# Performance work log

Hardware: AMD Instinct MI355X
Metric: run time of the kernel (lower is better)

## Reference

```python
import jax, jax.numpy as jnp
import numpy as np

NUM_EMB = 8192
EMB_DIM = 512
COMMITMENT_COST = 0.25
TEMPERATURE = 1.0
ENTROPY_WEIGHT = 0.1


def setup_inputs() -> dict:
    key = jax.random.key(0)
    k1, k2 = jax.random.split(key)
    z = jax.random.normal(k1, (32768, EMB_DIM), dtype=jnp.float32)
    W = jax.random.normal(k2, (NUM_EMB, EMB_DIM), dtype=jnp.float32) * 0.1
    return {"z": z, "W": W}


def reference(z, W):
    # pairwise squared distances [B, K] (scaled by temperature)
    distances = (jnp.sum(z * z, axis=1, keepdims=True)
                 + jnp.sum(W * W, axis=1)
                 - 2.0 * z @ W.T) / TEMPERATURE
    indices = jnp.argmin(distances, axis=1)          # [B]
    quantized = W[indices]                            # [B, D] gather

    commitment_loss = jnp.mean((z - jax.lax.stop_gradient(quantized)) ** 2)
    codebook_loss = jnp.mean((quantized - jax.lax.stop_gradient(z)) ** 2)

    # entropy loss over code assignment histogram
    counts = jnp.zeros((NUM_EMB,), jnp.float32).at[indices].add(1.0)
    probs = counts / jnp.maximum(counts.sum(), 1.0)
    entropy = -jnp.sum(probs * jnp.log(probs + 1e-10))
    max_entropy = jnp.log(jnp.float32(NUM_EMB))
    entropy_loss = 1.0 - entropy / max_entropy

    loss = codebook_loss + COMMITMENT_COST * commitment_loss + ENTROPY_WEIGHT * entropy_loss

    # straight-through estimator
    quantized_st = z + jax.lax.stop_gradient(quantized - z)
    return quantized_st, loss, indices
```

## Files before the change

kernel.cpp:

```cpp
#include <hip/hip_runtime.h>
#include <math.h>

#define B_ROWS 32768
#define D_DIM  512
#define K_EMB  8192

#define BMT 128
#define BNT 128
#define RSPLIT 16
#define KRANGE_R (K_EMB / RSPLIT)
#define EPS 0.10f

typedef __attribute__((ext_vector_type(4))) float f32x4;
typedef __attribute__((ext_vector_type(8))) short bf16x8;

#define GLL16(gp, lp)                                                          \
  __builtin_amdgcn_global_load_lds(                                            \
      (const __attribute__((address_space(1))) void*)(gp),                     \
      (__attribute__((address_space(3))) void*)(lp), 16, 0, 0)

__device__ __forceinline__ unsigned bf_rne(float x) {
  unsigned u = __float_as_uint(x);
  return (u + 0x7fffu + ((u >> 16) & 1u)) >> 16;
}

__global__ __launch_bounds__(256) void prep_kernel(
    const float* __restrict__ X, short* __restrict__ hi,
    short* __restrict__ lo, float* __restrict__ sq, int nrows) {
  const int wave = threadIdx.x >> 6;
  const int lane = threadIdx.x & 63;
  const int row = blockIdx.x * 4 + wave;
  if (row >= nrows) return;
  const float* xr = X + (size_t)row * D_DIM;
  float4 x0 = ((const float4*)xr)[lane * 2];
  float4 x1 = ((const float4*)xr)[lane * 2 + 1];
  float xs[8] = {x0.x, x0.y, x0.z, x0.w, x1.x, x1.y, x1.z, x1.w};
  union { short s[8]; int4 v; } H, L;
  float ssum = 0.f;
  #pragma unroll
  for (int j = 0; j < 8; ++j) {
    unsigned rh = bf_rne(xs[j]);
    H.s[j] = (short)rh;
    float h = __uint_as_float(rh << 16);
    L.s[j] = (short)bf_rne(xs[j] - h);
    ssum += xs[j] * xs[j];
  }
  *(int4*)(hi + (size_t)row * D_DIM + lane * 8) = H.v;
  *(int4*)(lo + (size_t)row * D_DIM + lane * 8) = L.v;
  #pragma unroll
  for (int o = 32; o > 0; o >>= 1) ssum += __shfl_xor(ssum, o, 64);
  if (lane == 0) sq[row] = ssum;
}

__global__ __launch_bounds__(512, 2) void stage1_kernel(
    const short* __restrict__ zhi, const short* __restrict__ whi,
    const float* __restrict__ wsq, float* __restrict__ cv1,
    int* __restrict__ ci1, float* __restrict__ cv2) {
  __shared__ short Zt[65536];
  float* rv1 = (float*)Zt;
  int*   ri1 = (int*)(Zt + 16384);
  float* rv2 = (float*)(Zt + 32768);

  const int tid = threadIdx.x;
  const int lane = tid & 63;
  const int wave = tid >> 6;
  const int wm = wave >> 2;
  const int wn = wave & 3;
  const int l15 = lane & 15, l4 = lane >> 4;
  const int row0 = blockIdx.x * 128;

  #pragma unroll
  for (int j = 0; j < 16; ++j) {
    const int slot = j * 512 + tid;
    const int r = slot & 127, dc = slot >> 7;
    GLL16(zhi + (size_t)(row0 + r) * D_DIM + dc * 8, Zt + (size_t)slot * 8);
  }

  const short* pb[4];
  #pragma unroll
  for (int cb = 0; cb < 4; ++cb)
    pb[cb] = whi + (size_t)(wn * 64 + cb * 16 + l15) * D_DIM + l4 * 8;

  float v1[16], v2[16];
  int   i1[16];
  #pragma unroll
  for (int s = 0; s < 16; ++s) { v1[s] = INFINITY; v2[s] = INFINITY; i1[s] = 0x7fffffff; }

  bf16x8 bcur[4];
  #pragma unroll
  for (int cb = 0; cb < 4; ++cb) bcur[cb] = *(const bf16x8*)(pb[cb]);

  __syncthreads();

  for (int kt = 0; kt < K_EMB; kt += 256) {
    f32x4 acc[4][4];
    #pragma unroll
    for (int rb = 0; rb < 4; ++rb)
      #pragma unroll
      for (int cb = 0; cb < 4; ++cb) acc[rb][cb] = (f32x4)0.f;

    #pragma unroll 4
    for (int dc = 0; dc < 16; ++dc) {
      const int nt0 = (dc == 15) ? kt + 256 : kt;
      const int nt = (nt0 < K_EMB) ? nt0 : 0;
      const int nd = (dc == 15) ? 0 : (dc + 1) * 32;
      const size_t noff = (size_t)nt * D_DIM + nd;
      bf16x8 bnxt[4];
      #pragma unroll
      for (int cb = 0; cb < 4; ++cb) bnxt[cb] = *(const bf16x8*)(pb[cb] + noff);

      bf16x8 a[4];
      #pragma unroll
      for (int rb = 0; rb < 4; ++rb)
        a[rb] = *(const bf16x8*)&Zt[((dc * 4 + l4) * 128 + wm * 64 + rb * 16 + l15) * 8];
      #pragma unroll
      for (int rb = 0; rb < 4; ++rb)
        #pragma unroll
        for (int cb = 0; cb < 4; ++cb)
          acc[rb][cb] = __builtin_amdgcn_mfma_f32_16x16x32_bf16(
              a[rb], bcur[cb], acc[rb][cb], 0, 0, 0);
      #pragma unroll
      for (int cb = 0; cb < 4; ++cb) bcur[cb] = bnxt[cb];
    }

    #pragma unroll
    for (int cb = 0; cb < 4; ++cb) {
      const int col = kt + wn * 64 + cb * 16 + l15;
      const float wv = wsq[col];
      #pragma unroll
      for (int rb = 0; rb < 4; ++rb) {
        f32x4 a = acc[rb][cb];
        #pragma unroll
        for (int rg = 0; rg < 4; ++rg) {
          const float dist = wv - 2.0f * a[rg];
          const int s = rb * 4 + rg;
          if (dist < v1[s]) {
            v2[s] = v1[s]; v1[s] = dist; i1[s] = col;
          } else {
            v2[s] = fminf(v2[s], dist);
          }
        }
      }
    }
  }

  __syncthreads();
  #pragma unroll
  for (int rb = 0; rb < 4; ++rb)
    #pragma unroll
    for (int rg = 0; rg < 4; ++rg) {
      const int s = rb * 4 + rg;
      const int R = wm * 64 + rb * 16 + l4 * 4 + rg;
      const int c = wn * 16 + l15;
      rv1[R * 64 + c] = v1[s];
      ri1[R * 64 + c] = i1[s];
      rv2[R * 64 + c] = v2[s];
    }
  __syncthreads();

  if (tid < 128) {
    float V1 = INFINITY, V2 = INFINITY;
    int I1 = 0x7fffffff;
    #pragma unroll 8
    for (int t = 0; t < 64; ++t) {
      const float a1 = rv1[tid * 64 + t];
      const int ai = ri1[tid * 64 + t];
      const float a2 = rv2[tid * 64 + t];
      if (a1 < V1 || (a1 == V1 && ai < I1)) {
        V2 = fminf(V1, a2); V1 = a1; I1 = ai;
      } else {
        V2 = fminf(V2, a1);
      }
    }
    cv1[row0 + tid] = V1; ci1[row0 + tid] = I1; cv2[row0 + tid] = V2;
  }
}

__global__ __launch_bounds__(256) void merge_flag_kernel(
    const float* __restrict__ cv1, const int* __restrict__ ci1,
    const float* __restrict__ cv2, int* __restrict__ idx,
    float* __restrict__ out_idx_f, int* __restrict__ hist,
    unsigned long long* __restrict__ packed, int* __restrict__ cnt,
    int* __restrict__ list) {
  const int row = blockIdx.x * 256 + threadIdx.x;
  const float V1 = cv1[row];
  const int I1 = ci1[row];
  const float V2 = cv2[row];
  if (V2 - V1 >= EPS) {
    idx[row] = I1;
    out_idx_f[row] = (float)I1;
    atomicAdd(&hist[I1], 1);
  } else {
    packed[row] = 0xffffffffffffffffULL;
    const int p = atomicAdd(cnt, 1);
    list[p] = row;
  }
}

__global__ __launch_bounds__(256, 2) void refine_kernel(
    const short* __restrict__ zhi, const short* __restrict__ zlo,
    const short* __restrict__ whi, const short* __restrict__ wlo,
    const float* __restrict__ zz, const float* __restrict__ wsq,
    const int* __restrict__ cnt, const int* __restrict__ list,
    unsigned long long* __restrict__ packed) {
  __shared__ char smem[32768];
  short* Ah = (short*)smem;
  short* Al = (short*)(smem + 8192);
  short* Bh = (short*)(smem + 16384);
  short* Bl = (short*)(smem + 24576);
  float* rv = (float*)smem;
  int*   ri = (int*)(smem + 16384);

  const int n = *cnt;
  const int bx = blockIdx.x;
  const int rt = bx >> 4;
  const int ks = bx & 15;
  if (rt * BMT >= n) return;
  const int k0 = ks * KRANGE_R;

  const int tid = threadIdx.x;
  const int lane = tid & 63;
  const int wave = tid >> 6;
  const int wm = wave >> 1, wn = wave & 1;
  const int l15 = lane & 15, l4 = lane >> 4;

  const int r0s = tid & 127;
  const int kc0 = tid >> 7;
  const int kc1 = kc0 + 2;
  const int rowg = list[min(rt * BMT + r0s, n - 1)];

  float zzr[16];
  #pragma unroll
  for (int rb = 0; rb < 4; ++rb)
    #pragma unroll
    for (int rg = 0; rg < 4; ++rg) {
      const int m = wm * 64 + rb * 16 + l4 * 4 + rg;
      zzr[rb * 4 + rg] = zz[list[min(rt * BMT + m, n - 1)]];
    }

  float best[16];
  int   bidx[16];
  #pragma unroll
  for (int s = 0; s < 16; ++s) { best[s] = INFINITY; bidx[s] = 0x7fffffff; }

  for (int kt = 0; kt < KRANGE_R; kt += BNT) {
    f32x4 acc[4][4];
    #pragma unroll
    for (int rb = 0; rb < 4; ++rb)
      #pragma unroll
      for (int cb = 0; cb < 4; ++cb) acc[rb][cb] = (f32x4)0.f;

    for (int d0 = 0; d0 < D_DIM; d0 += 32) {
      const size_t ga0 = (size_t)rowg * D_DIM + d0 + kc0 * 8;
      const size_t ga1 = (size_t)rowg * D_DIM + d0 + kc1 * 8;
      const size_t gb0 = (size_t)(k0 + kt + r0s) * D_DIM + d0 + kc0 * 8;
      const size_t gb1 = (size_t)(k0 + kt + r0s) * D_DIM + d0 + kc1 * 8;
      GLL16(zhi + ga0, Ah + (size_t)tid * 8);
      GLL16(zhi + ga1, Ah + (size_t)(tid + 256) * 8);
      GLL16(zlo + ga0, Al + (size_t)tid * 8);
      GLL16(zlo + ga1, Al + (size_t)(tid + 256) * 8);
      GLL16(whi + gb0, Bh + (size_t)tid * 8);
      GLL16(whi + gb1, Bh + (size_t)(tid + 256) * 8);
      GLL16(wlo + gb0, Bl + (size_t)tid * 8);
      GLL16(wlo + gb1, Bl + (size_t)(tid + 256) * 8);
      __syncthreads();

      bf16x8 ah[4], al[4], bh[4], bl[4];
      #pragma unroll
      for (int rb = 0; rb < 4; ++rb) {
        const int m = wm * 64 + rb * 16 + l15;
        ah[rb] = *(const bf16x8*)&Ah[(l4 * 128 + m) * 8];
        al[rb] = *(const bf16x8*)&Al[(l4 * 128 + m) * 8];
      }
      #pragma unroll
      for (int cb = 0; cb < 4; ++cb) {
        const int nn = wn * 64 + cb * 16 + l15;
        bh[cb] = *(const bf16x8*)&Bh[(l4 * 128 + nn) * 8];
        bl[cb] = *(const bf16x8*)&Bl[(l4 * 128 + nn) * 8];
      }
      #pragma unroll
      for (int rb = 0; rb < 4; ++rb)
        #pragma unroll
        for (int cb = 0; cb < 4; ++cb) {
          acc[rb][cb] = __builtin_amdgcn_mfma_f32_16x16x32_bf16(
              ah[rb], bh[cb], acc[rb][cb], 0, 0, 0);
          acc[rb][cb] = __builtin_amdgcn_mfma_f32_16x16x32_bf16(
              ah[rb], bl[cb], acc[rb][cb], 0, 0, 0);
          acc[rb][cb] = __builtin_amdgcn_mfma_f32_16x16x32_bf16(
              al[rb], bh[cb], acc[rb][cb], 0, 0, 0);
        }
      __syncthreads();
    }

    #pragma unroll
    for (int cb = 0; cb < 4; ++cb) {
      const int col = k0 + kt + wn * 64 + cb * 16 + l15;
      const float wv = wsq[col];
      #pragma unroll
      for (int rb = 0; rb < 4; ++rb) {
        f32x4 a = acc[rb][cb];
        #pragma unroll
        for (int rg = 0; rg < 4; ++rg) {
          const float dist = (zzr[rb * 4 + rg] + wv) - 2.0f * a[rg];
          const int s = rb * 4 + rg;
          if (dist < best[s]) { best[s] = dist; bidx[s] = col; }
        }
      }
    }
  }

  #pragma unroll
  for (int rb = 0; rb < 4; ++rb)
    #pragma unroll
    for (int rg = 0; rg < 4; ++rg) {
      const int s = rb * 4 + rg;
      const int R = wm * 64 + rb * 16 + l4 * 4 + rg;
      rv[R * 32 + wn * 16 + l15] = best[s];
      ri[R * 32 + wn * 16 + l15] = bidx[s];
    }
  __syncthreads();

  if (tid < BMT && rt * BMT + tid < n) {
    float bv = INFINITY;
    int bi = 0x7fffffff;
    #pragma unroll
    for (int t = 0; t < 32; ++t) {
      const float v = rv[tid * 32 + t];
      const int ix = ri[tid * 32 + t];
      if (v < bv || (v == bv && ix < bi)) { bv = v; bi = ix; }
    }
    const int row = list[rt * BMT + tid];
    const unsigned long long pk =
        ((unsigned long long)__float_as_uint(bv) << 32) | (unsigned)bi;
    atomicMin(&packed[row], pk);
  }
}

__global__ __launch_bounds__(256) void final_merge_kernel(
    const int* __restrict__ cnt, const int* __restrict__ list,
    const unsigned long long* __restrict__ packed, int* __restrict__ idx,
    float* __restrict__ out_idx_f, int* __restrict__ hist) {
  const int t = blockIdx.x * 256 + threadIdx.x;
  if (t >= *cnt) return;
  const int row = list[t];
  const int bi = (int)(packed[row] & 0xffffffffULL);
  idx[row] = bi;
  out_idx_f[row] = (float)bi;
  atomicAdd(&hist[bi], 1);
}

__global__ __launch_bounds__(256) void gather_kernel(
    const float* __restrict__ z, const float* __restrict__ W,
    const int* __restrict__ idx, float* __restrict__ out,
    double* __restrict__ mse_part) {
  __shared__ float wsum[4];
  const int wave = threadIdx.x >> 6;
  const int lane = threadIdx.x & 63;
  const int row = blockIdx.x * 4 + wave;
  const int k = idx[row];
  const float* zr = z + (size_t)row * D_DIM;
  const float* wr = W + (size_t)k * D_DIM;
  float* outr = out + (size_t)row * D_DIM;
  float s = 0.f;
  #pragma unroll
  for (int h = 0; h < 2; ++h) {
    const int c = h * 256 + lane * 4;
    float4 zv = *(const float4*)(zr + c);
    float4 qv = *(const float4*)(wr + c);
    float4 st;
    st.x = zv.x + (qv.x - zv.x);
    st.y = zv.y + (qv.y - zv.y);
    st.z = zv.z + (qv.z - zv.z);
    st.w = zv.w + (qv.w - zv.w);
    float dx = zv.x - qv.x, dy = zv.y - qv.y, dz = zv.z - qv.z, dw = zv.w - qv.w;
    s += dx * dx + dy * dy + dz * dz + dw * dw;
    *(float4*)(outr + c) = st;
  }
  #pragma unroll
  for (int o = 32; o > 0; o >>= 1) s += __shfl_xor(s, o, 64);
  if (lane == 0) wsum[wave] = s;
  __syncthreads();
  if (threadIdx.x == 0)
    mse_part[blockIdx.x] =
        (double)wsum[0] + (double)wsum[1] + (double)wsum[2] + (double)wsum[3];
}

__global__ __launch_bounds__(256) void loss_kernel(
    const int* __restrict__ hist, const double* __restrict__ mse_part,
    float* __restrict__ out_loss) {
  __shared__ float ls[4];
  __shared__ double ld[4];
  const int tid = threadIdx.x;
  float e = 0.f;
  double ms = 0.0;
  for (int b = tid; b < K_EMB; b += 256) {
    float p = (float)hist[b] * (1.0f / 32768.0f);
    e += p * logf(p + 1e-10f);
    ms += mse_part[b];
  }
  #pragma unroll
  for (int o = 32; o > 0; o >>= 1) {
    e += __shfl_xor(e, o, 64);
    ms += __shfl_xor(ms, o, 64);
  }
  if ((tid & 63) == 0) { ls[tid >> 6] = e; ld[tid >> 6] = ms; }
  __syncthreads();
  if (tid == 0) {
    float entropy = -(ls[0] + ls[1] + ls[2] + ls[3]);
    float mse = (float)((ld[0] + ld[1] + ld[2] + ld[3]) / 16777216.0);
    float entropy_loss = 1.0f - entropy / logf(8192.0f);
    out_loss[0] = mse + 0.25f * mse + 0.1f * entropy_loss;
  }
}

extern "C" void kernel_launch(void* const* d_in, const int* in_sizes, int n_in,
                              void* d_out, int out_size, void* d_ws, size_t ws_size,
                              hipStream_t stream) {
  const float* z = (const float*)d_in[0];
  const float* W = (const float*)d_in[1];
  float* out = (float*)d_out;

  char* ws = (char*)d_ws;
  int*    cnt     = (int*)(ws + 8);
  int*    hist    = (int*)(ws + 4096);
  unsigned long long* packed = (unsigned long long*)(ws + 65536);
  float*  zz   = (float*)(ws + 327680);
  float*  wsq  = (float*)(ws + 458752);
  int*    idx  = (int*)(ws + 491520);
  int*    list = (int*)(ws + 622592);
  float*  cv1  = (float*)(ws + 786432);
  int*    ci1  = (int*)(ws + 1310720);
  float*  cv2  = (float*)(ws + 1835008);
  double* mse_part = (double*)(ws + 2097152);
  short*  zhi  = (short*)(ws + 4194304);
  short*  zlo  = (short*)(ws + 37748736);
  short*  whi  = (short*)(ws + 71303168);
  short*  wlo  = (short*)(ws + 79691776);

  hipMemsetAsync(d_ws, 0, 36864, stream);

  prep_kernel<<<B_ROWS / 4, 256, 0, stream>>>(z, zhi, zlo, zz, B_ROWS);
  prep_kernel<<<K_EMB / 4, 256, 0, stream>>>(W, whi, wlo, wsq, K_EMB);

  stage1_kernel<<<B_ROWS / 128, 512, 0, stream>>>(zhi, whi, wsq, cv1, ci1, cv2);

  merge_flag_kernel<<<B_ROWS / 256, 256, 0, stream>>>(
      cv1, ci1, cv2, idx, out + (size_t)B_ROWS * D_DIM + 1, hist,
      packed, cnt, list);

  refine_kernel<<<(B_ROWS / BMT) * RSPLIT, 256, 0, stream>>>(
      zhi, zlo, whi, wlo, zz, wsq, cnt, list, packed);

  final_merge_kernel<<<B_ROWS / 256, 256, 0, stream>>>(
      cnt, list, packed, idx, out + (size_t)B_ROWS * D_DIM + 1, hist);

  gather_kernel<<<B_ROWS / 4, 256, 0, stream>>>(z, W, idx, out, mse_part);

  loss_kernel<<<1, 256, 0, stream>>>(hist, mse_part,
                                     out + (size_t)B_ROWS * D_DIM);
}
```

Before: 807.0 us.

## Shrink stage1 block tile to 64 rows and reduce top-2 via wave shuffles

The stage1 distance/argmin kernel now handles 64 query rows per block instead of 128, with each of 8 waves owning 32 codebook columns per 256-column tile. This halves LDS use and accumulator registers, so launch bounds can allow 4 blocks per CU and there are twice as many blocks. The cross-lane top-2 reduction becomes a shuffle butterfly within each wave followed by a small 8-way LDS merge, replacing the large LDS scratch scan. In exchange, each block loads the W tiles for half as many rows, doubling global/L2 traffic for the codebook, and per-wave MFMA work per load drops.

```diff
diff --git a/kernel.cpp b/kernel.cpp
--- a/kernel.cpp
+++ b/kernel.cpp
@@ -52,52 +52,50 @@
   if (lane == 0) sq[row] = ssum;
 }
 
-__global__ __launch_bounds__(512, 2) void stage1_kernel(
+__global__ __launch_bounds__(512, 4) void stage1_kernel(
     const short* __restrict__ zhi, const short* __restrict__ whi,
     const float* __restrict__ wsq, float* __restrict__ cv1,
     int* __restrict__ ci1, float* __restrict__ cv2) {
-  __shared__ short Zt[65536];
+  __shared__ short Zt[32768];
   float* rv1 = (float*)Zt;
-  int*   ri1 = (int*)(Zt + 16384);
-  float* rv2 = (float*)(Zt + 32768);
+  int*   ri1 = (int*)(Zt + 1024);
+  float* rv2 = (float*)(Zt + 2048);
 
   const int tid = threadIdx.x;
   const int lane = tid & 63;
   const int wave = tid >> 6;
-  const int wm = wave >> 2;
-  const int wn = wave & 3;
   const int l15 = lane & 15, l4 = lane >> 4;
-  const int row0 = blockIdx.x * 128;
-
-  #pragma unroll
-  for (int j = 0; j < 16; ++j) {
+  const int row0 = blockIdx.x * 64;
+
+  #pragma unroll
+  for (int j = 0; j < 8; ++j) {
     const int slot = j * 512 + tid;
-    const int r = slot & 127, dc = slot >> 7;
+    const int r = slot & 63, dc = slot >> 6;
     GLL16(zhi + (size_t)(row0 + r) * D_DIM + dc * 8, Zt + (size_t)slot * 8);
   }
 
-  const short* pb[4];
-  #pragma unroll
-  for (int cb = 0; cb < 4; ++cb)
-    pb[cb] = whi + (size_t)(wn * 64 + cb * 16 + l15) * D_DIM + l4 * 8;
+  const short* pb[2];
+  #pragma unroll
+  for (int cb = 0; cb < 2; ++cb)
+    pb[cb] = whi + (size_t)(wave * 32 + cb * 16 + l15) * D_DIM + l4 * 8;
 
   float v1[16], v2[16];
   int   i1[16];
   #pragma unroll
   for (int s = 0; s < 16; ++s) { v1[s] = INFINITY; v2[s] = INFINITY; i1[s] = 0x7fffffff; }
 
-  bf16x8 bcur[4];
-  #pragma unroll
-  for (int cb = 0; cb < 4; ++cb) bcur[cb] = *(const bf16x8*)(pb[cb]);
+  bf16x8 bcur[2];
+  #pragma unroll
+  for (int cb = 0; cb < 2; ++cb) bcur[cb] = *(const bf16x8*)(pb[cb]);
 
   __syncthreads();
 
   for (int kt = 0; kt < K_EMB; kt += 256) {
-    f32x4 acc[4][4];
+    f32x4 acc[4][2];
     #pragma unroll
     for (int rb = 0; rb < 4; ++rb)
       #pragma unroll
-      for (int cb = 0; cb < 4; ++cb) acc[rb][cb] = (f32x4)0.f;
+      for (int cb = 0; cb < 2; ++cb) acc[rb][cb] = (f32x4)0.f;
 
     #pragma unroll 4
     for (int dc = 0; dc < 16; ++dc) {
@@ -105,27 +103,27 @@
       const int nt = (nt0 < K_EMB) ? nt0 : 0;
       const int nd = (dc == 15) ? 0 : (dc + 1) * 32;
       const size_t noff = (size_t)nt * D_DIM + nd;
-      bf16x8 bnxt[4];
-      #pragma unroll
-      for (int cb = 0; cb < 4; ++cb) bnxt[cb] = *(const bf16x8*)(pb[cb] + noff);
+      bf16x8 bnxt[2];
+      #pragma unroll
+      for (int cb = 0; cb < 2; ++cb) bnxt[cb] = *(const bf16x8*)(pb[cb] + noff);
 
       bf16x8 a[4];
       #pragma unroll
       for (int rb = 0; rb < 4; ++rb)
-        a[rb] = *(const bf16x8*)&Zt[((dc * 4 + l4) * 128 + wm * 64 + rb * 16 + l15) * 8];
+        a[rb] = *(const bf16x8*)&Zt[((dc * 4 + l4) * 64 + rb * 16 + l15) * 8];
       #pragma unroll
       for (int rb = 0; rb < 4; ++rb)
         #pragma unroll
-        for (int cb = 0; cb < 4; ++cb)
+        for (int cb = 0; cb < 2; ++cb)
           acc[rb][cb] = __builtin_amdgcn_mfma_f32_16x16x32_bf16(
               a[rb], bcur[cb], acc[rb][cb], 0, 0, 0);
       #pragma unroll
-      for (int cb = 0; cb < 4; ++cb) bcur[cb] = bnxt[cb];
-    }
-
-    #pragma unroll
-    for (int cb = 0; cb < 4; ++cb) {
-      const int col = kt + wn * 64 + cb * 16 + l15;
+      for (int cb = 0; cb < 2; ++cb) bcur[cb] = bnxt[cb];
+    }
+
+    #pragma unroll
+    for (int cb = 0; cb < 2; ++cb) {
+      const int col = kt + wave * 32 + cb * 16 + l15;
       const float wv = wsq[col];
       #pragma unroll
       for (int rb = 0; rb < 4; ++rb) {
@@ -146,26 +144,37 @@
 
   __syncthreads();
   #pragma unroll
-  for (int rb = 0; rb < 4; ++rb)
-    #pragma unroll
-    for (int rg = 0; rg < 4; ++rg) {
-      const int s = rb * 4 + rg;
-      const int R = wm * 64 + rb * 16 + l4 * 4 + rg;
-      const int c = wn * 16 + l15;
-      rv1[R * 64 + c] = v1[s];
-      ri1[R * 64 + c] = i1[s];
-      rv2[R * 64 + c] = v2[s];
-    }
-  __syncthreads();
-
-  if (tid < 128) {
+  for (int s = 0; s < 16; ++s) {
+    float a1 = v1[s], a2 = v2[s];
+    int ai = i1[s];
+    #pragma unroll
+    for (int m = 1; m < 16; m <<= 1) {
+      const float b1 = __shfl_xor(a1, m, 64);
+      const float b2 = __shfl_xor(a2, m, 64);
+      const int   bi = __shfl_xor(ai, m, 64);
+      if (b1 < a1 || (b1 == a1 && bi < ai)) {
+        a2 = fminf(a1, b2); a1 = b1; ai = bi;
+      } else {
+        a2 = fminf(a2, b1);
+      }
+    }
+    if (l15 == 0) {
+      const int r = (s >> 2) * 16 + l4 * 4 + (s & 3);
+      rv1[r * 8 + wave] = a1;
+      ri1[r * 8 + wave] = ai;
+      rv2[r * 8 + wave] = a2;
+    }
+  }
+  __syncthreads();
+
+  if (tid < 64) {
     float V1 = INFINITY, V2 = INFINITY;
     int I1 = 0x7fffffff;
-    #pragma unroll 8
-    for (int t = 0; t < 64; ++t) {
-      const float a1 = rv1[tid * 64 + t];
-      const int ai = ri1[tid * 64 + t];
-      const float a2 = rv2[tid * 64 + t];
+    #pragma unroll
+    for (int w = 0; w < 8; ++w) {
+      const float a1 = rv1[tid * 8 + w];
+      const int ai = ri1[tid * 8 + w];
+      const float a2 = rv2[tid * 8 + w];
       if (a1 < V1 || (a1 == V1 && ai < I1)) {
         V2 = fminf(V1, a2); V1 = a1; I1 = ai;
       } else {
@@ -442,7 +451,7 @@
   prep_kernel<<<B_ROWS / 4, 256, 0, stream>>>(z, zhi, zlo, zz, B_ROWS);
   prep_kernel<<<K_EMB / 4, 256, 0, stream>>>(W, whi, wlo, wsq, K_EMB);
 
-  stage1_kernel<<<B_ROWS / 128, 512, 0, stream>>>(zhi, whi, wsq, cv1, ci1, cv2);
+  stage1_kernel<<<B_ROWS / 64, 512, 0, stream>>>(zhi, whi, wsq, cv1, ci1, cv2);
 
   merge_flag_kernel<<<B_ROWS / 256, 256, 0, stream>>>(
       cv1, ci1, cv2, idx, out + (size_t)B_ROWS * D_DIM + 1, hist,
```

Measured after the change: 803.0 us. Within noise of the previous version (-0.5%).

## Split stage1 codebook range across block groups with LDS-staged tiles and merge kernel

Applied to the files above, without the earlier changes.

Restructures the bf16 distance GEMM. Each block now covers 128 rows against a quarter of the codebook, staging both Z and W k-slices through LDS with global_load_lds, instead of holding all of Z in LDS and streaming W directly from global per wave. The grid grows from 256 to 1024 blocks of 256 threads, with a swizzled block order so blocks sharing W tiles run together. Per-tile top-2 is reduced with cross-lane shuffles, and a new small kernel merges the four group partials per row. The aim is more parallelism and occupancy, in exchange for two barriers per k-step with no double buffering and an extra kernel launch plus partial-result traffic.

```diff
diff --git a/kernel.cpp b/kernel.cpp
--- a/kernel.cpp
+++ b/kernel.cpp
@@ -10,6 +10,9 @@
 #define RSPLIT 16
 #define KRANGE_R (K_EMB / RSPLIT)
 #define EPS 0.10f
+
+#define S1_NG  4
+#define S1_TPG 16
 
 typedef __attribute__((ext_vector_type(4))) float f32x4;
 typedef __attribute__((ext_vector_type(8))) short bf16x8;
@@ -52,128 +55,150 @@
   if (lane == 0) sq[row] = ssum;
 }
 
-__global__ __launch_bounds__(512, 2) void stage1_kernel(
+__global__ __launch_bounds__(256, 3) void stage1_gemm(
     const short* __restrict__ zhi, const short* __restrict__ whi,
-    const float* __restrict__ wsq, float* __restrict__ cv1,
-    int* __restrict__ ci1, float* __restrict__ cv2) {
-  __shared__ short Zt[65536];
-  float* rv1 = (float*)Zt;
-  int*   ri1 = (int*)(Zt + 16384);
-  float* rv2 = (float*)(Zt + 32768);
+    const float* __restrict__ wsq, float* __restrict__ cgv1,
+    int* __restrict__ cgi1, float* __restrict__ cgv2) {
+  __shared__ short As[4096];
+  __shared__ short Bs[4096];
+  __shared__ float ctv1[256];
+  __shared__ int   cti1[256];
+  __shared__ float ctv2[256];
 
   const int tid = threadIdx.x;
   const int lane = tid & 63;
   const int wave = tid >> 6;
-  const int wm = wave >> 2;
-  const int wn = wave & 3;
+  const int wm = wave >> 1, wn = wave & 1;
   const int l15 = lane & 15, l4 = lane >> 4;
-  const int row0 = blockIdx.x * 128;
-
-  #pragma unroll
-  for (int j = 0; j < 16; ++j) {
-    const int slot = j * 512 + tid;
-    const int r = slot & 127, dc = slot >> 7;
-    GLL16(zhi + (size_t)(row0 + r) * D_DIM + dc * 8, Zt + (size_t)slot * 8);
-  }
-
-  const short* pb[4];
-  #pragma unroll
-  for (int cb = 0; cb < 4; ++cb)
-    pb[cb] = whi + (size_t)(wn * 64 + cb * 16 + l15) * D_DIM + l4 * 8;
-
-  float v1[16], v2[16];
-  int   i1[16];
-  #pragma unroll
-  for (int s = 0; s < 16; ++s) { v1[s] = INFINITY; v2[s] = INFINITY; i1[s] = 0x7fffffff; }
-
-  bf16x8 bcur[4];
-  #pragma unroll
-  for (int cb = 0; cb < 4; ++cb) bcur[cb] = *(const bf16x8*)(pb[cb]);
-
-  __syncthreads();
-
-  for (int kt = 0; kt < K_EMB; kt += 256) {
+
+  const int wg = ((blockIdx.x & 7) << 7) | (blockIdx.x >> 3);
+  const int g = wg >> 8;
+  const int mt = wg & 255;
+  const int row0 = mt * 128;
+
+  const int r_st = tid & 127;
+  const int d_st = tid >> 7;
+
+  float rv1 = INFINITY, rv2 = INFINITY;
+  int   ri1 = 0x7fffffff;
+
+  for (int nt = 0; nt < S1_TPG; ++nt) {
+    const int kb = (g * S1_TPG + nt) * 128;
     f32x4 acc[4][4];
     #pragma unroll
     for (int rb = 0; rb < 4; ++rb)
       #pragma unroll
       for (int cb = 0; cb < 4; ++cb) acc[rb][cb] = (f32x4)0.f;
 
-    #pragma unroll 4
-    for (int dc = 0; dc < 16; ++dc) {
-      const int nt0 = (dc == 15) ? kt + 256 : kt;
-      const int nt = (nt0 < K_EMB) ? nt0 : 0;
-      const int nd = (dc == 15) ? 0 : (dc + 1) * 32;
-      const size_t noff = (size_t)nt * D_DIM + nd;
-      bf16x8 bnxt[4];
-      #pragma unroll
-      for (int cb = 0; cb < 4; ++cb) bnxt[cb] = *(const bf16x8*)(pb[cb] + noff);
-
-      bf16x8 a[4];
+    for (int ks = 0; ks < 16; ++ks) {
+      const int d0 = ks * 32;
+      const size_t ga = (size_t)(row0 + r_st) * D_DIM + d0 + d_st * 8;
+      const size_t gb = (size_t)(kb + r_st) * D_DIM + d0 + d_st * 8;
+      GLL16(zhi + ga,      As + (size_t)tid * 8);
+      GLL16(zhi + ga + 16, As + (size_t)(tid + 256) * 8);
+      GLL16(whi + gb,      Bs + (size_t)tid * 8);
+      GLL16(whi + gb + 16, Bs + (size_t)(tid + 256) * 8);
+      __syncthreads();
+
+      bf16x8 a[4], b[4];
       #pragma unroll
       for (int rb = 0; rb < 4; ++rb)
-        a[rb] = *(const bf16x8*)&Zt[((dc * 4 + l4) * 128 + wm * 64 + rb * 16 + l15) * 8];
+        a[rb] = *(const bf16x8*)&As[(l4 * 128 + wm * 64 + rb * 16 + l15) * 8];
+      #pragma unroll
+      for (int cb = 0; cb < 4; ++cb)
+        b[cb] = *(const bf16x8*)&Bs[(l4 * 128 + wn * 64 + cb * 16 + l15) * 8];
       #pragma unroll
       for (int rb = 0; rb < 4; ++rb)
         #pragma unroll
         for (int cb = 0; cb < 4; ++cb)
           acc[rb][cb] = __builtin_amdgcn_mfma_f32_16x16x32_bf16(
-              a[rb], bcur[cb], acc[rb][cb], 0, 0, 0);
-      #pragma unroll
-      for (int cb = 0; cb < 4; ++cb) bcur[cb] = bnxt[cb];
-    }
-
+              a[rb], b[cb], acc[rb][cb], 0, 0, 0);
+      __syncthreads();
+    }
+
+    float wvv[4]; int colv[4];
     #pragma unroll
     for (int cb = 0; cb < 4; ++cb) {
-      const int col = kt + wn * 64 + cb * 16 + l15;
-      const float wv = wsq[col];
-      #pragma unroll
-      for (int rb = 0; rb < 4; ++rb) {
-        f32x4 a = acc[rb][cb];
+      colv[cb] = kb + wn * 64 + cb * 16 + l15;
+      wvv[cb] = wsq[colv[cb]];
+    }
+    #pragma unroll
+    for (int rb = 0; rb < 4; ++rb)
+      #pragma unroll
+      for (int rg = 0; rg < 4; ++rg) {
+        float tv1 = INFINITY, tv2 = INFINITY;
+        int ti1 = 0x7fffffff;
         #pragma unroll
-        for (int rg = 0; rg < 4; ++rg) {
-          const float dist = wv - 2.0f * a[rg];
-          const int s = rb * 4 + rg;
-          if (dist < v1[s]) {
-            v2[s] = v1[s]; v1[s] = dist; i1[s] = col;
+        for (int cb = 0; cb < 4; ++cb) {
+          const float dist = wvv[cb] - 2.0f * acc[rb][cb][rg];
+          if (dist < tv1) { tv2 = tv1; tv1 = dist; ti1 = colv[cb]; }
+          else tv2 = fminf(tv2, dist);
+        }
+        #pragma unroll
+        for (int m = 1; m < 16; m <<= 1) {
+          const float b1 = __shfl_xor(tv1, m, 64);
+          const float b2 = __shfl_xor(tv2, m, 64);
+          const int   bi = __shfl_xor(ti1, m, 64);
+          if (b1 < tv1 || (b1 == tv1 && bi < ti1)) {
+            tv2 = fminf(tv1, b2); tv1 = b1; ti1 = bi;
           } else {
-            v2[s] = fminf(v2[s], dist);
+            tv2 = fminf(tv2, b1);
           }
         }
+        if (l15 == 0) {
+          const int r = wm * 64 + rb * 16 + l4 * 4 + rg;
+          ctv1[r * 2 + wn] = tv1;
+          cti1[r * 2 + wn] = ti1;
+          ctv2[r * 2 + wn] = tv2;
+        }
       }
-    }
-  }
-
-  __syncthreads();
-  #pragma unroll
-  for (int rb = 0; rb < 4; ++rb)
-    #pragma unroll
-    for (int rg = 0; rg < 4; ++rg) {
-      const int s = rb * 4 + rg;
-      const int R = wm * 64 + rb * 16 + l4 * 4 + rg;
-      const int c = wn * 16 + l15;
-      rv1[R * 64 + c] = v1[s];
-      ri1[R * 64 + c] = i1[s];
-      rv2[R * 64 + c] = v2[s];
-    }
-  __syncthreads();
+    __syncthreads();
+    if (tid < 128) {
+      #pragma unroll
+      for (int h = 0; h < 2; ++h) {
+        const float b1 = ctv1[tid * 2 + h];
+        const float b2 = ctv2[tid * 2 + h];
+        const int   bi = cti1[tid * 2 + h];
+        if (b1 < rv1 || (b1 == rv1 && bi < ri1)) {
+          rv2 = fminf(rv1, b2); rv1 = b1; ri1 = bi;
+        } else {
+          rv2 = fminf(rv2, b1);
+        }
+      }
+    }
+    __syncthreads();
+  }
 
   if (tid < 128) {
-    float V1 = INFINITY, V2 = INFINITY;
-    int I1 = 0x7fffffff;
-    #pragma unroll 8
-    for (int t = 0; t < 64; ++t) {
-      const float a1 = rv1[tid * 64 + t];
-      const int ai = ri1[tid * 64 + t];
-      const float a2 = rv2[tid * 64 + t];
-      if (a1 < V1 || (a1 == V1 && ai < I1)) {
-        V2 = fminf(V1, a2); V1 = a1; I1 = ai;
-      } else {
-        V2 = fminf(V2, a1);
-      }
-    }
-    cv1[row0 + tid] = V1; ci1[row0 + tid] = I1; cv2[row0 + tid] = V2;
-  }
+    const int o = (row0 + tid) * S1_NG + g;
+    cgv1[o] = rv1; cgi1[o] = ri1; cgv2[o] = rv2;
+  }
+}
+
+__global__ __launch_bounds__(256) void merge_groups_kernel(
+    const float* __restrict__ cgv1, const int* __restrict__ cgi1,
+    const float* __restrict__ cgv2, float* __restrict__ cv1,
+    int* __restrict__ ci1, float* __restrict__ cv2) {
+  const int row = blockIdx.x * 256 + threadIdx.x;
+  const float4 q1 = ((const float4*)cgv1)[row];
+  const int4   qi = ((const int4*)cgi1)[row];
+  const float4 q2 = ((const float4*)cgv2)[row];
+  float V1 = q1.x, V2 = q2.x;
+  int I1 = qi.x;
+  const float b1s[3] = {q1.y, q1.z, q1.w};
+  const float b2s[3] = {q2.y, q2.z, q2.w};
+  const int   bis[3] = {qi.y, qi.z, qi.w};
+  #pragma unroll
+  for (int gg = 0; gg < 3; ++gg) {
+    const float b1 = b1s[gg], b2 = b2s[gg];
+    const int bi = bis[gg];
+    if (b1 < V1 || (b1 == V1 && bi < I1)) {
+      V2 = fminf(V1, b2); V1 = b1; I1 = bi;
+    } else {
+      V2 = fminf(V2, b1);
+    }
+  }
+  cv1[row] = V1; ci1[row] = I1; cv2[row] = V2;
 }
 
 __global__ __launch_bounds__(256) void merge_flag_kernel(
@@ -432,6 +457,9 @@
   int*    ci1  = (int*)(ws + 1310720);
   float*  cv2  = (float*)(ws + 1835008);
   double* mse_part = (double*)(ws + 2097152);
+  float*  cgv1 = (float*)(ws + 2162688);
+  int*    cgi1 = (int*)(ws + 2686976);
+  float*  cgv2 = (float*)(ws + 3211264);
   short*  zhi  = (short*)(ws + 4194304);
   short*  zlo  = (short*)(ws + 37748736);
   short*  whi  = (short*)(ws + 71303168);
@@ -442,7 +470,10 @@
   prep_kernel<<<B_ROWS / 4, 256, 0, stream>>>(z, zhi, zlo, zz, B_ROWS);
   prep_kernel<<<K_EMB / 4, 256, 0, stream>>>(W, whi, wlo, wsq, K_EMB);
 
-  stage1_kernel<<<B_ROWS / 128, 512, 0, stream>>>(zhi, whi, wsq, cv1, ci1, cv2);
+  stage1_gemm<<<256 * S1_NG, 256, 0, stream>>>(zhi, whi, wsq, cgv1, cgi1, cgv2);
+
+  merge_groups_kernel<<<B_ROWS / 256, 256, 0, stream>>>(
+      cgv1, cgi1, cgv2, cv1, ci1, cv2);
 
   merge_flag_kernel<<<B_ROWS / 256, 256, 0, stream>>>(
       cv1, ci1, cv2, idx, out + (size_t)B_ROWS * D_DIM + 1, hist,
```

Result: slower. 1.365 ms (+69.1%).
